# Performance work log

Hardware: AMD Instinct MI355X
Metric: run time of the kernel (lower is better)

## Reference

```python
import jax, jax.numpy as jnp
import numpy as np

N_NODES = 100000

def graph_conv(x, edge_index, w_root, w_rel, b):
    # PyG GraphConv (aggr='add'): out = aggr(x_j) @ W_rel + b + x @ W_root
    src, dst = edge_index[0], edge_index[1]
    msgs = x[src]                                   # [E, F_in] gather
    agg = jax.ops.segment_sum(msgs, dst, num_segments=N_NODES)  # [N, F_in] scatter-add
    return agg @ w_rel + b + x @ w_root             # [N, F_out]


def setup_inputs() -> dict:
    key = jax.random.key(0)
    ks = jax.random.split(key, 12)
    E = 1600000
    return {
        "x": jax.random.normal(ks[0], (N_NODES, 16), dtype=jnp.float32),
        "edge_index": jax.random.randint(ks[1], (2, E), 0, N_NODES, dtype=jnp.int64),
        "w_root1": jax.random.normal(ks[2], (16, 32), dtype=jnp.float32) * 0.1,
        "w_rel1": jax.random.normal(ks[3], (16, 32), dtype=jnp.float32) * 0.1,
        "b1": jax.random.normal(ks[4], (32,), dtype=jnp.float32) * 0.1,
        "w_root2": jax.random.normal(ks[5], (32, 64), dtype=jnp.float32) * 0.1,
        "w_rel2": jax.random.normal(ks[6], (32, 64), dtype=jnp.float32) * 0.1,
        "b2": jax.random.normal(ks[7], (64,), dtype=jnp.float32) * 0.1,
        "fc1_w": jax.random.normal(ks[8], (64, 32), dtype=jnp.float32) * 0.1,
        "fc1_b": jax.random.normal(ks[9], (32,), dtype=jnp.float32) * 0.1,
        "fc2_w": jax.random.normal(ks[10], (32, 16), dtype=jnp.float32) * 0.1,
        "fc2_b": jax.random.normal(ks[11], (16,), dtype=jnp.float32) * 0.1,
    }


def reference(x, edge_index, w_root1, w_rel1, b1, w_root2, w_rel2, b2,
              fc1_w, fc1_b, fc2_w, fc2_b):
    h = jax.nn.relu(graph_conv(x, edge_index, w_root1, w_rel1, b1))   # [N, 32]
    h = jax.nn.relu(graph_conv(h, edge_index, w_root2, w_rel2, b2))   # [N, 64]
    h = jax.nn.relu(h @ fc1_w + fc1_b)                                 # [N, 32]
    return h @ fc2_w + fc2_b                                           # [N, 16]
```

## Files before the change

### kernel.cpp

```cpp
#include <hip/hip_runtime.h>

#define F4E(v,i) ((i)==0?(v).x:((i)==1?(v).y:((i)==2?(v).z:(v).w)))

#define CHUNK 4096
#define ITERS 8

__device__ inline float4 shfl4b(float4 v, int src) {
    float4 r;
    r.x = __shfl(v.x, src, 4); r.y = __shfl(v.y, src, 4);
    r.z = __shfl(v.z, src, 4); r.w = __shfl(v.w, src, 4);
    return r;
}
__device__ inline float4 shfl8b(float4 v, int src) {
    float4 r;
    r.x = __shfl(v.x, src, 8); r.y = __shfl(v.y, src, 8);
    r.z = __shfl(v.z, src, 8); r.w = __shfl(v.w, src, 8);
    return r;
}

__global__ __launch_bounds__(512) void k_bhist(
    const int* __restrict__ ei, int* __restrict__ bhist, int E, int NB)
{
    __shared__ int cnt[512];
    int t = threadIdx.x;
    cnt[t] = 0;
    __syncthreads();
    int base = blockIdx.x * CHUNK;
#pragma unroll
    for (int i = 0; i < ITERS; ++i) {
        int e = base + i * 512 + t;
        if (e < E) {
            int dst = ei[E + e];
            atomicAdd(&cnt[dst >> 8], 1);
        }
    }
    __syncthreads();
    if (t < NB && cnt[t]) atomicAdd(&bhist[t], cnt[t]);
}

__global__ __launch_bounds__(512) void k_bscan(
    const int* __restrict__ bhist, int* __restrict__ bstart,
    int* __restrict__ gcursor, int NB, int E)
{
    __shared__ int s[512];
    int t = threadIdx.x;
    int v0 = (t < NB) ? bhist[t] : 0;
    s[t] = v0;
    __syncthreads();
    for (int off = 1; off < 512; off <<= 1) {
        int v = (t >= off) ? s[t - off] : 0;
        __syncthreads();
        s[t] += v;
        __syncthreads();
    }
    if (t < NB) { int ex = s[t] - v0; bstart[t] = ex; gcursor[t] = ex; }
    if (t == 0) bstart[NB] = E;
}

__global__ __launch_bounds__(512) void k_partition(
    const int* __restrict__ ei, int* __restrict__ gcursor,
    int* __restrict__ epack, int E)
{
    __shared__ int cnt[512], sc[512], lbase[512], gbase[512], lcnt[512];
    __shared__ int stage[CHUNK];
    __shared__ unsigned short stageb[CHUNK];
    int t = threadIdx.x;
    cnt[t] = 0; lcnt[t] = 0;
    __syncthreads();

    int base = blockIdx.x * CHUNK;
    int pk[ITERS], bb[ITERS];
#pragma unroll
    for (int i = 0; i < ITERS; ++i) {
        int e = base + i * 512 + t;
        if (e < E) {
            int src = ei[e], dst = ei[E + e];
            pk[i] = (src << 8) | (dst & 255);
            bb[i] = dst >> 8;
            atomicAdd(&cnt[bb[i]], 1);
        } else bb[i] = -1;
    }
    __syncthreads();

    int v0 = cnt[t];
    sc[t] = v0;
    __syncthreads();
    for (int off = 1; off < 512; off <<= 1) {
        int v = (t >= off) ? sc[t - off] : 0;
        __syncthreads();
        sc[t] += v;
        __syncthreads();
    }
    lbase[t] = sc[t] - v0;
    if (v0 > 0) gbase[t] = atomicAdd(&gcursor[t], v0);
    __syncthreads();

#pragma unroll
    for (int i = 0; i < ITERS; ++i) {
        if (bb[i] >= 0) {
            int loc = atomicAdd(&lcnt[bb[i]], 1);
            int slot = lbase[bb[i]] + loc;
            stage[slot] = pk[i];
            stageb[slot] = (unsigned short)bb[i];
        }
    }
    __syncthreads();

    int m = min(CHUNK, E - base);
#pragma unroll
    for (int i = 0; i < ITERS; ++i) {
        int slot = i * 512 + t;
        if (slot < m) {
            int b = stageb[slot];
            epack[gbase[b] + (slot - lbase[b])] = stage[slot];
        }
    }
}

__global__ __launch_bounds__(256) void k_sort(
    const int* __restrict__ bstart, const int* __restrict__ epack,
    int* __restrict__ rs, int* __restrict__ esorted, int N, int E)
{
    __shared__ int hist[256], cur[256], sc[256];
    int t = threadIdx.x;
    int b = blockIdx.x;
    int s0 = bstart[b], s1 = bstart[b + 1];
    hist[t] = 0;
    __syncthreads();
    for (int e = s0 + t; e < s1; e += 256)
        atomicAdd(&hist[epack[e] & 255], 1);
    __syncthreads();

    int v0 = hist[t];
    sc[t] = v0;
    __syncthreads();
    for (int off = 1; off < 256; off <<= 1) {
        int v = (t >= off) ? sc[t - off] : 0;
        __syncthreads();
        sc[t] += v;
        __syncthreads();
    }
    int excl = sc[t] - v0;
    cur[t] = excl;
    int node = (b << 8) + t;
    if (node < N) rs[node] = s0 + excl;
    if (b == 0 && t == 0) rs[N] = E;
    __syncthreads();

    for (int e = s0 + t; e < s1; e += 256) {
        int pk = epack[e];
        int dlo = pk & 255;
        int pos = s0 + atomicAdd(&cur[dlo], 1);
        esorted[pos] = ((unsigned)pk) >> 8;
    }
}

__global__ __launch_bounds__(256) void k_g1f(
    const float* __restrict__ x, const int* __restrict__ rs,
    const int* __restrict__ esrc,
    const float* __restrict__ wroot, const float* __restrict__ wrel,
    const float* __restrict__ bias, float* __restrict__ h1, int N)
{
    __shared__ float4 s_wr[128], s_wl[128], s_b[8];
    int t = threadIdx.x;
    if (t < 128) {
        s_wr[t] = reinterpret_cast<const float4*>(wroot)[t];
        s_wl[t] = reinterpret_cast<const float4*>(wrel)[t];
    }
    if (t < 8) s_b[t] = reinterpret_cast<const float4*>(bias)[t];
    __syncthreads();

    int tid = blockIdx.x * 256 + t;
    int n = tid >> 2, p = tid & 3;
    if (n >= N) return;
    int s0 = rs[n], s1 = rs[n + 1];
    float4 g = make_float4(0.f, 0.f, 0.f, 0.f);
    int e = s0;
    for (; e + 1 < s1; e += 2) {
        int src0 = esrc[e], src1 = esrc[e + 1];
        float4 v0 = *reinterpret_cast<const float4*>(x + (size_t)src0 * 16 + p * 4);
        float4 v1 = *reinterpret_cast<const float4*>(x + (size_t)src1 * 16 + p * 4);
        g.x += v0.x + v1.x; g.y += v0.y + v1.y;
        g.z += v0.z + v1.z; g.w += v0.w + v1.w;
    }
    if (e < s1) {
        int src0 = esrc[e];
        float4 v0 = *reinterpret_cast<const float4*>(x + (size_t)src0 * 16 + p * 4);
        g.x += v0.x; g.y += v0.y; g.z += v0.z; g.w += v0.w;
    }
    float4 a = *reinterpret_cast<const float4*>(x + (size_t)n * 16 + p * 4);

    int jb = p * 2;
    float4 acc0 = s_b[jb], acc1 = s_b[jb + 1];
#pragma unroll
    for (int kc = 0; kc < 4; ++kc) {
        float4 a4 = shfl4b(a, kc);
        float4 g4 = shfl4b(g, kc);
#pragma unroll
        for (int kk = 0; kk < 4; ++kk) {
            float av = F4E(a4, kk), gv = F4E(g4, kk);
            int k = kc * 4 + kk;
            float4 wr0 = s_wr[k * 8 + jb], wr1 = s_wr[k * 8 + jb + 1];
            float4 wl0 = s_wl[k * 8 + jb], wl1 = s_wl[k * 8 + jb + 1];
            acc0.x += av * wr0.x + gv * wl0.x;
            acc0.y += av * wr0.y + gv * wl0.y;
            acc0.z += av * wr0.z + gv * wl0.z;
            acc0.w += av * wr0.w + gv * wl0.w;
            acc1.x += av * wr1.x + gv * wl1.x;
            acc1.y += av * wr1.y + gv * wl1.y;
            acc1.z += av * wr1.z + gv * wl1.z;
            acc1.w += av * wr1.w + gv * wl1.w;
        }
    }
    acc0.x = fmaxf(acc0.x, 0.f); acc0.y = fmaxf(acc0.y, 0.f);
    acc0.z = fmaxf(acc0.z, 0.f); acc0.w = fmaxf(acc0.w, 0.f);
    acc1.x = fmaxf(acc1.x, 0.f); acc1.y = fmaxf(acc1.y, 0.f);
    acc1.z = fmaxf(acc1.z, 0.f); acc1.w = fmaxf(acc1.w, 0.f);
    float4* o = reinterpret_cast<float4*>(h1 + (size_t)n * 32 + p * 8);
    o[0] = acc0; o[1] = acc1;
}

__global__ __launch_bounds__(256) void k_g2f(
    const float* __restrict__ h1, const int* __restrict__ rs,
    const int* __restrict__ esrc,
    const float* __restrict__ wroot, const float* __restrict__ wrel,
    const float* __restrict__ bias,
    const float* __restrict__ f1w, const float* __restrict__ f1b,
    const float* __restrict__ f2w, const float* __restrict__ f2b,
    float* __restrict__ out, int N)
{
    __shared__ float4 s_wr[512], s_wl[512], s_b[16];
    __shared__ float4 s_f1[512];
    __shared__ float  s_f2[512];
    __shared__ float4 s_b1[8];
    __shared__ float  s_b2[16];
    int t = threadIdx.x;
    for (int i = t; i < 512; i += 256) {
        s_wr[i] = reinterpret_cast<const float4*>(wroot)[i];
        s_wl[i] = reinterpret_cast<const float4*>(wrel)[i];
        int k = i >> 3, jc = i & 7;
        s_f1[(i & ~7) | ((jc + (k >> 3)) & 7)] = reinterpret_cast<const float4*>(f1w)[i];
        s_f2[i] = f2w[i];
    }
    if (t < 16) s_b[t]  = reinterpret_cast<const float4*>(bias)[t];
    if (t < 8)  s_b1[t] = reinterpret_cast<const float4*>(f1b)[t];
    if (t < 16) s_b2[t] = f2b[t];
    __syncthreads();

    int tid = blockIdx.x * 256 + t;
    int n = tid >> 3, p = tid & 7;
    if (n >= N) return;

    int s0 = rs[n], s1 = rs[n + 1];
    float4 g = make_float4(0.f, 0.f, 0.f, 0.f);
    int e = s0;
    for (; e + 1 < s1; e += 2) {
        int src0 = esrc[e], src1 = esrc[e + 1];
        float4 v0 = *reinterpret_cast<const float4*>(h1 + (size_t)src0 * 32 + p * 4);
        float4 v1 = *reinterpret_cast<const float4*>(h1 + (size_t)src1 * 32 + p * 4);
        g.x += v0.x + v1.x; g.y += v0.y + v1.y;
        g.z += v0.z + v1.z; g.w += v0.w + v1.w;
    }
    if (e < s1) {
        int src0 = esrc[e];
        float4 v0 = *reinterpret_cast<const float4*>(h1 + (size_t)src0 * 32 + p * 4);
        g.x += v0.x; g.y += v0.y; g.z += v0.z; g.w += v0.w;
    }
    float4 a = *reinterpret_cast<const float4*>(h1 + (size_t)n * 32 + p * 4);

    int jb = p * 2;
    float4 acc0 = s_b[jb], acc1 = s_b[jb + 1];
#pragma unroll
    for (int kc = 0; kc < 8; ++kc) {
        float4 a4 = shfl8b(a, kc);
        float4 g4 = shfl8b(g, kc);
#pragma unroll
        for (int kk = 0; kk < 4; ++kk) {
            float av = F4E(a4, kk), gv = F4E(g4, kk);
            int k = kc * 4 + kk;
            float4 wr0 = s_wr[k * 16 + jb], wr1 = s_wr[k * 16 + jb + 1];
            float4 wl0 = s_wl[k * 16 + jb], wl1 = s_wl[k * 16 + jb + 1];
            acc0.x += av * wr0.x + gv * wl0.x;
            acc0.y += av * wr0.y + gv * wl0.y;
            acc0.z += av * wr0.z + gv * wl0.z;
            acc0.w += av * wr0.w + gv * wl0.w;
            acc1.x += av * wr1.x + gv * wl1.x;
            acc1.y += av * wr1.y + gv * wl1.y;
            acc1.z += av * wr1.z + gv * wl1.z;
            acc1.w += av * wr1.w + gv * wl1.w;
        }
    }
    acc0.x = fmaxf(acc0.x, 0.f); acc0.y = fmaxf(acc0.y, 0.f);
    acc0.z = fmaxf(acc0.z, 0.f); acc0.w = fmaxf(acc0.w, 0.f);
    acc1.x = fmaxf(acc1.x, 0.f); acc1.y = fmaxf(acc1.y, 0.f);
    acc1.z = fmaxf(acc1.z, 0.f); acc1.w = fmaxf(acc1.w, 0.f);

    float4 f[8];
    float4 z4 = make_float4(0.f, 0.f, 0.f, 0.f);
#pragma unroll
    for (int jc = 0; jc < 8; ++jc) f[jc] = p ? z4 : s_b1[jc];
#pragma unroll
    for (int kk = 0; kk < 8; ++kk) {
        float hv = (kk < 4) ? F4E(acc0, kk) : F4E(acc1, kk - 4);
        int k = p * 8 + kk;
        int row = k * 8;
#pragma unroll
        for (int jc = 0; jc < 8; ++jc) {
            float4 w = s_f1[row | ((jc + p) & 7)];
            f[jc].x += hv * w.x; f[jc].y += hv * w.y;
            f[jc].z += hv * w.z; f[jc].w += hv * w.w;
        }
    }
#pragma unroll
    for (int m = 1; m < 8; m <<= 1) {
#pragma unroll
        for (int jc = 0; jc < 8; ++jc) {
            f[jc].x += __shfl_xor(f[jc].x, m);
            f[jc].y += __shfl_xor(f[jc].y, m);
            f[jc].z += __shfl_xor(f[jc].z, m);
            f[jc].w += __shfl_xor(f[jc].w, m);
        }
    }
#pragma unroll
    for (int jc = 0; jc < 8; ++jc) {
        f[jc].x = fmaxf(f[jc].x, 0.f); f[jc].y = fmaxf(f[jc].y, 0.f);
        f[jc].z = fmaxf(f[jc].z, 0.f); f[jc].w = fmaxf(f[jc].w, 0.f);
    }

    float o0 = s_b2[p * 2], o1 = s_b2[p * 2 + 1];
#pragma unroll
    for (int k2 = 0; k2 < 32; ++k2) {
        float av = F4E(f[k2 >> 2], k2 & 3);
        o0 += av * s_f2[k2 * 16 + p * 2];
        o1 += av * s_f2[k2 * 16 + p * 2 + 1];
    }
    float2* o = reinterpret_cast<float2*>(out + (size_t)n * 16 + p * 2);
    *o = make_float2(o0, o1);
}

extern "C" void kernel_launch(void* const* d_in, const int* in_sizes, int n_in,
                              void* d_out, int out_size, void* d_ws, size_t ws_size,
                              hipStream_t stream)
{
    const float* x   = (const float*)d_in[0];
    const int*   ei  = (const int*)d_in[1];
    const float* wr1 = (const float*)d_in[2];
    const float* wl1 = (const float*)d_in[3];
    const float* b1  = (const float*)d_in[4];
    const float* wr2 = (const float*)d_in[5];
    const float* wl2 = (const float*)d_in[6];
    const float* b2  = (const float*)d_in[7];
    const float* f1w = (const float*)d_in[8];
    const float* f1b = (const float*)d_in[9];
    const float* f2w = (const float*)d_in[10];
    const float* f2b = (const float*)d_in[11];
    float* out = (float*)d_out;

    const int N  = in_sizes[0] / 16;
    const int E  = in_sizes[1] / 2;
    const int NB = (N + 255) >> 8;

    float* ws      = (float*)d_ws;
    float* h1      = ws;
    int*   esorted = (int*)(ws + (size_t)N * 32);
    int*   epack   = esorted + E;
    int*   rs      = epack + E;
    int*   bhist   = rs + N + 1;
    int*   bstart  = bhist + NB;
    int*   gcursor = bstart + NB + 1;

    hipMemsetAsync(bhist, 0, (size_t)NB * sizeof(int), stream);

    int nchunk = (E + CHUNK - 1) / CHUNK;
    int g_g1 = (N * 4 + 255) / 256;
    int g_g2 = (N * 8 + 255) / 256;

    k_bhist    <<<nchunk, 512, 0, stream>>>(ei, bhist, E, NB);
    k_bscan    <<<1,      512, 0, stream>>>(bhist, bstart, gcursor, NB, E);
    k_partition<<<nchunk, 512, 0, stream>>>(ei, gcursor, epack, E);
    k_sort     <<<NB,     256, 0, stream>>>(bstart, epack, rs, esorted, N, E);

    k_g1f      <<<g_g1, 256, 0, stream>>>(x, rs, esorted, wr1, wl1, b1, h1, N);
    k_g2f      <<<g_g2, 256, 0, stream>>>(h1, rs, esorted, wr2, wl2, b2,
                                          f1w, f1b, f2w, f2b, out, N);
}
```

Before: 229.5 us.

## Bin nodes by in-degree into a permutation to balance gather-loop work per wavefront

Counts node in-degrees into 64 bins during the per-bucket sort and adds a kernel that builds a degree-sorted node permutation. Both GraphConv kernels then walk nodes in that order, so lanes in a wavefront have similar loop trip counts and divergence drops. The gather loops are also unrolled from 2 to 4 edges to keep more loads in flight. In exchange it adds an extra kernel launch, global atomics on 64 counters, an indirection load per node, and scattered output writes and root-row reads because neighbouring threads no longer handle neighbouring nodes.

New measurement: 800.2 us. 3.49x slower.

```diff
diff --git a/kernel.cpp b/kernel.cpp
--- a/kernel.cpp
+++ b/kernel.cpp
@@ -119,7 +119,8 @@
 
 __global__ __launch_bounds__(256) void k_sort(
     const int* __restrict__ bstart, const int* __restrict__ epack,
-    int* __restrict__ rs, int* __restrict__ esorted, int N, int E)
+    int* __restrict__ rs, int* __restrict__ esorted,
+    int* __restrict__ dcnt, int N, int E)
 {
     __shared__ int hist[256], cur[256], sc[256];
     int t = threadIdx.x;
@@ -143,7 +144,10 @@
     int excl = sc[t] - v0;
     cur[t] = excl;
     int node = (b << 8) + t;
-    if (node < N) rs[node] = s0 + excl;
+    if (node < N) {
+        rs[node] = s0 + excl;
+        atomicAdd(&dcnt[min(v0, 63)], 1);
+    }
     if (b == 0 && t == 0) rs[N] = E;
     __syncthreads();
 
@@ -155,9 +159,34 @@
     }
 }
 
+__global__ __launch_bounds__(256) void k_perm(
+    const int* __restrict__ rs, const int* __restrict__ dcnt,
+    int* __restrict__ dcur, int* __restrict__ perm, int N)
+{
+    __shared__ int sstart[64];
+    int t = threadIdx.x;
+    if (t < 64) {
+        int v = dcnt[t];
+        int incl = v;
+#pragma unroll
+        for (int d = 1; d < 64; d <<= 1) {
+            int o = __shfl_up(incl, d, 64);
+            if (t >= d) incl += o;
+        }
+        sstart[t] = incl - v;
+    }
+    __syncthreads();
+    int node = blockIdx.x * 256 + t;
+    if (node >= N) return;
+    int deg = rs[node + 1] - rs[node];
+    int bin = min(deg, 63);
+    int pos = sstart[bin] + atomicAdd(&dcur[bin], 1);
+    perm[pos] = node;
+}
+
 __global__ __launch_bounds__(256) void k_g1f(
     const float* __restrict__ x, const int* __restrict__ rs,
-    const int* __restrict__ esrc,
+    const int* __restrict__ esrc, const int* __restrict__ perm,
     const float* __restrict__ wroot, const float* __restrict__ wrel,
     const float* __restrict__ bias, float* __restrict__ h1, int N)
 {
@@ -171,21 +200,26 @@
     __syncthreads();
 
     int tid = blockIdx.x * 256 + t;
-    int n = tid >> 2, p = tid & 3;
-    if (n >= N) return;
+    int q = tid >> 2, p = tid & 3;
+    if (q >= N) return;
+    int n = perm[q];
     int s0 = rs[n], s1 = rs[n + 1];
     float4 g = make_float4(0.f, 0.f, 0.f, 0.f);
     int e = s0;
-    for (; e + 1 < s1; e += 2) {
-        int src0 = esrc[e], src1 = esrc[e + 1];
-        float4 v0 = *reinterpret_cast<const float4*>(x + (size_t)src0 * 16 + p * 4);
-        float4 v1 = *reinterpret_cast<const float4*>(x + (size_t)src1 * 16 + p * 4);
-        g.x += v0.x + v1.x; g.y += v0.y + v1.y;
-        g.z += v0.z + v1.z; g.w += v0.w + v1.w;
-    }
-    if (e < s1) {
-        int src0 = esrc[e];
-        float4 v0 = *reinterpret_cast<const float4*>(x + (size_t)src0 * 16 + p * 4);
+    for (; e + 3 < s1; e += 4) {
+        int sa = esrc[e], sb = esrc[e + 1], sc = esrc[e + 2], sd = esrc[e + 3];
+        float4 v0 = *reinterpret_cast<const float4*>(x + (size_t)sa * 16 + p * 4);
+        float4 v1 = *reinterpret_cast<const float4*>(x + (size_t)sb * 16 + p * 4);
+        float4 v2 = *reinterpret_cast<const float4*>(x + (size_t)sc * 16 + p * 4);
+        float4 v3 = *reinterpret_cast<const float4*>(x + (size_t)sd * 16 + p * 4);
+        g.x += (v0.x + v1.x) + (v2.x + v3.x);
+        g.y += (v0.y + v1.y) + (v2.y + v3.y);
+        g.z += (v0.z + v1.z) + (v2.z + v3.z);
+        g.w += (v0.w + v1.w) + (v2.w + v3.w);
+    }
+    for (; e < s1; ++e) {
+        int sa = esrc[e];
+        float4 v0 = *reinterpret_cast<const float4*>(x + (size_t)sa * 16 + p * 4);
         g.x += v0.x; g.y += v0.y; g.z += v0.z; g.w += v0.w;
     }
     float4 a = *reinterpret_cast<const float4*>(x + (size_t)n * 16 + p * 4);
@@ -222,7 +256,7 @@
 
 __global__ __launch_bounds__(256) void k_g2f(
     const float* __restrict__ h1, const int* __restrict__ rs,
-    const int* __restrict__ esrc,
+    const int* __restrict__ esrc, const int* __restrict__ perm,
     const float* __restrict__ wroot, const float* __restrict__ wrel,
     const float* __restrict__ bias,
     const float* __restrict__ f1w, const float* __restrict__ f1b,
@@ -248,22 +282,27 @@
     __syncthreads();
 
     int tid = blockIdx.x * 256 + t;
-    int n = tid >> 3, p = tid & 7;
-    if (n >= N) return;
+    int q = tid >> 3, p = tid & 7;
+    if (q >= N) return;
+    int n = perm[q];
 
     int s0 = rs[n], s1 = rs[n + 1];
     float4 g = make_float4(0.f, 0.f, 0.f, 0.f);
     int e = s0;
-    for (; e + 1 < s1; e += 2) {
-        int src0 = esrc[e], src1 = esrc[e + 1];
-        float4 v0 = *reinterpret_cast<const float4*>(h1 + (size_t)src0 * 32 + p * 4);
-        float4 v1 = *reinterpret_cast<const float4*>(h1 + (size_t)src1 * 32 + p * 4);
-        g.x += v0.x + v1.x; g.y += v0.y + v1.y;
-        g.z += v0.z + v1.z; g.w += v0.w + v1.w;
-    }
-    if (e < s1) {
-        int src0 = esrc[e];
-        float4 v0 = *reinterpret_cast<const float4*>(h1 + (size_t)src0 * 32 + p * 4);
+    for (; e + 3 < s1; e += 4) {
+        int sa = esrc[e], sb = esrc[e + 1], sc = esrc[e + 2], sd = esrc[e + 3];
+        float4 v0 = *reinterpret_cast<const float4*>(h1 + (size_t)sa * 32 + p * 4);
+        float4 v1 = *reinterpret_cast<const float4*>(h1 + (size_t)sb * 32 + p * 4);
+        float4 v2 = *reinterpret_cast<const float4*>(h1 + (size_t)sc * 32 + p * 4);
+        float4 v3 = *reinterpret_cast<const float4*>(h1 + (size_t)sd * 32 + p * 4);
+        g.x += (v0.x + v1.x) + (v2.x + v3.x);
+        g.y += (v0.y + v1.y) + (v2.y + v3.y);
+        g.z += (v0.z + v1.z) + (v2.z + v3.z);
+        g.w += (v0.w + v1.w) + (v2.w + v3.w);
+    }
+    for (; e < s1; ++e) {
+        int sa = esrc[e];
+        float4 v0 = *reinterpret_cast<const float4*>(h1 + (size_t)sa * 32 + p * 4);
         g.x += v0.x; g.y += v0.y; g.z += v0.z; g.w += v0.w;
     }
     float4 a = *reinterpret_cast<const float4*>(h1 + (size_t)n * 32 + p * 4);
@@ -366,21 +405,28 @@
     int*   epack   = esorted + E;
     int*   rs      = epack + E;
     int*   bhist   = rs + N + 1;
-    int*   bstart  = bhist + NB;
+    int*   dcnt    = bhist + NB;
+    int*   dcur    = dcnt + 64;
+    int*   bstart  = dcur + 64;
     int*   gcursor = bstart + NB + 1;
-
-    hipMemsetAsync(bhist, 0, (size_t)NB * sizeof(int), stream);
+    int*   perm    = gcursor + NB;
+
+    hipMemsetAsync(bhist, 0, (size_t)(NB + 128) * sizeof(int), stream);
 
     int nchunk = (E + CHUNK - 1) / CHUNK;
+    int g_n  = (N + 255) / 256;
     int g_g1 = (N * 4 + 255) / 256;
     int g_g2 = (N * 8 + 255) / 256;
 
     k_bhist    <<<nchunk, 512, 0, stream>>>(ei, bhist, E, NB);
     k_bscan    <<<1,      512, 0, stream>>>(bhist, bstart, gcursor, NB, E);
     k_partition<<<nchunk, 512, 0, stream>>>(ei, gcursor, epack, E);
-    k_sort     <<<NB,     256, 0, stream>>>(bstart, epack, rs, esorted, N, E);
-
-    k_g1f      <<<g_g1, 256, 0, stream>>>(x, rs, esorted, wr1, wl1, b1, h1, N);
-    k_g2f      <<<g_g2, 256, 0, stream>>>(h1, rs, esorted, wr2, wl2, b2,
+    k_sort     <<<NB,     256, 0, stream>>>(bstart, epack, rs, esorted, dcnt, N, E);
+    k_perm     <<<g_n,    256, 0, stream>>>(rs, dcnt, dcur, perm, N);
+
+    k_g1f      <<<g_g1, 256, 0, stream>>>(x, rs, esorted, perm,
+                                          wr1, wl1, b1, h1, N);
+    k_g2f      <<<g_g2, 256, 0, stream>>>(h1, rs, esorted, perm,
+                                          wr2, wl2, b2,
                                           f1w, f1b, f2w, f2b, out, N);
 }
```

## Store intermediate h1 as bf16 and unroll gather loops by eight

Applied to the files above, without the earlier changes.

The layer-1 output h1 is now written as packed bf16 with round-to-nearest-even, which halves the bytes the layer-2 gather reads per edge. Both gather loops are unrolled to issue eight independent loads before accumulating, to raise memory-level parallelism. The cost is lost precision in h1 and more registers per thread, which could reduce occupancy.

Result: faster. 220.6 us (-3.9%).

```diff
diff --git a/kernel.cpp b/kernel.cpp
--- a/kernel.cpp
+++ b/kernel.cpp
@@ -17,6 +17,15 @@
     r.z = __shfl(v.z, src, 8); r.w = __shfl(v.w, src, 8);
     return r;
 }
+
+__device__ inline unsigned packbf2(float a, float b) {
+    unsigned ua = __float_as_uint(a), ub = __float_as_uint(b);
+    ua = (ua + 0x7fffu + ((ua >> 16) & 1u)) >> 16;
+    ub = (ub + 0x7fffu + ((ub >> 16) & 1u)) >> 16;
+    return ua | (ub << 16);
+}
+__device__ inline float bflo(unsigned w) { return __uint_as_float(w << 16); }
+__device__ inline float bfhi(unsigned w) { return __uint_as_float(w & 0xffff0000u); }
 
 __global__ __launch_bounds__(512) void k_bhist(
     const int* __restrict__ ei, int* __restrict__ bhist, int E, int NB)
@@ -159,7 +168,7 @@
     const float* __restrict__ x, const int* __restrict__ rs,
     const int* __restrict__ esrc,
     const float* __restrict__ wroot, const float* __restrict__ wrel,
-    const float* __restrict__ bias, float* __restrict__ h1, int N)
+    const float* __restrict__ bias, unsigned short* __restrict__ h1, int N)
 {
     __shared__ float4 s_wr[128], s_wl[128], s_b[8];
     int t = threadIdx.x;
@@ -176,16 +185,21 @@
     int s0 = rs[n], s1 = rs[n + 1];
     float4 g = make_float4(0.f, 0.f, 0.f, 0.f);
     int e = s0;
-    for (; e + 1 < s1; e += 2) {
-        int src0 = esrc[e], src1 = esrc[e + 1];
-        float4 v0 = *reinterpret_cast<const float4*>(x + (size_t)src0 * 16 + p * 4);
-        float4 v1 = *reinterpret_cast<const float4*>(x + (size_t)src1 * 16 + p * 4);
-        g.x += v0.x + v1.x; g.y += v0.y + v1.y;
-        g.z += v0.z + v1.z; g.w += v0.w + v1.w;
-    }
-    if (e < s1) {
-        int src0 = esrc[e];
-        float4 v0 = *reinterpret_cast<const float4*>(x + (size_t)src0 * 16 + p * 4);
+    for (; e + 7 < s1; e += 8) {
+        float4 v[8];
+#pragma unroll
+        for (int u = 0; u < 8; ++u) {
+            int src = esrc[e + u];
+            v[u] = *reinterpret_cast<const float4*>(x + (size_t)src * 16 + p * 4);
+        }
+#pragma unroll
+        for (int u = 0; u < 8; ++u) {
+            g.x += v[u].x; g.y += v[u].y; g.z += v[u].z; g.w += v[u].w;
+        }
+    }
+    for (; e < s1; ++e) {
+        int src = esrc[e];
+        float4 v0 = *reinterpret_cast<const float4*>(x + (size_t)src * 16 + p * 4);
         g.x += v0.x; g.y += v0.y; g.z += v0.z; g.w += v0.w;
     }
     float4 a = *reinterpret_cast<const float4*>(x + (size_t)n * 16 + p * 4);
@@ -216,12 +230,17 @@
     acc0.z = fmaxf(acc0.z, 0.f); acc0.w = fmaxf(acc0.w, 0.f);
     acc1.x = fmaxf(acc1.x, 0.f); acc1.y = fmaxf(acc1.y, 0.f);
     acc1.z = fmaxf(acc1.z, 0.f); acc1.w = fmaxf(acc1.w, 0.f);
-    float4* o = reinterpret_cast<float4*>(h1 + (size_t)n * 32 + p * 8);
-    o[0] = acc0; o[1] = acc1;
+
+    uint4 w;
+    w.x = packbf2(acc0.x, acc0.y);
+    w.y = packbf2(acc0.z, acc0.w);
+    w.z = packbf2(acc1.x, acc1.y);
+    w.w = packbf2(acc1.z, acc1.w);
+    reinterpret_cast<uint4*>(h1 + (size_t)n * 32)[p] = w;
 }
 
 __global__ __launch_bounds__(256) void k_g2f(
-    const float* __restrict__ h1, const int* __restrict__ rs,
+    const unsigned short* __restrict__ h1, const int* __restrict__ rs,
     const int* __restrict__ esrc,
     const float* __restrict__ wroot, const float* __restrict__ wrel,
     const float* __restrict__ bias,
@@ -254,19 +273,27 @@
     int s0 = rs[n], s1 = rs[n + 1];
     float4 g = make_float4(0.f, 0.f, 0.f, 0.f);
     int e = s0;
-    for (; e + 1 < s1; e += 2) {
-        int src0 = esrc[e], src1 = esrc[e + 1];
-        float4 v0 = *reinterpret_cast<const float4*>(h1 + (size_t)src0 * 32 + p * 4);
-        float4 v1 = *reinterpret_cast<const float4*>(h1 + (size_t)src1 * 32 + p * 4);
-        g.x += v0.x + v1.x; g.y += v0.y + v1.y;
-        g.z += v0.z + v1.z; g.w += v0.w + v1.w;
-    }
-    if (e < s1) {
-        int src0 = esrc[e];
-        float4 v0 = *reinterpret_cast<const float4*>(h1 + (size_t)src0 * 32 + p * 4);
-        g.x += v0.x; g.y += v0.y; g.z += v0.z; g.w += v0.w;
-    }
-    float4 a = *reinterpret_cast<const float4*>(h1 + (size_t)n * 32 + p * 4);
+    for (; e + 7 < s1; e += 8) {
+        uint2 w[8];
+#pragma unroll
+        for (int u = 0; u < 8; ++u) {
+            int src = esrc[e + u];
+            w[u] = reinterpret_cast<const uint2*>(h1 + (size_t)src * 32)[p];
+        }
+#pragma unroll
+        for (int u = 0; u < 8; ++u) {
+            g.x += bflo(w[u].x); g.y += bfhi(w[u].x);
+            g.z += bflo(w[u].y); g.w += bfhi(w[u].y);
+        }
+    }
+    for (; e < s1; ++e) {
+        int src = esrc[e];
+        uint2 w0 = reinterpret_cast<const uint2*>(h1 + (size_t)src * 32)[p];
+        g.x += bflo(w0.x); g.y += bfhi(w0.x);
+        g.z += bflo(w0.y); g.w += bfhi(w0.y);
+    }
+    uint2 aw = reinterpret_cast<const uint2*>(h1 + (size_t)n * 32)[p];
+    float4 a = make_float4(bflo(aw.x), bfhi(aw.x), bflo(aw.y), bfhi(aw.y));
 
     int jb = p * 2;
     float4 acc0 = s_b[jb], acc1 = s_b[jb + 1];
@@ -360,14 +387,14 @@
     const int E  = in_sizes[1] / 2;
     const int NB = (N + 255) >> 8;
 
-    float* ws      = (float*)d_ws;
-    float* h1      = ws;
-    int*   esorted = (int*)(ws + (size_t)N * 32);
-    int*   epack   = esorted + E;
-    int*   rs      = epack + E;
-    int*   bhist   = rs + N + 1;
-    int*   bstart  = bhist + NB;
-    int*   gcursor = bstart + NB + 1;
+    float*          ws      = (float*)d_ws;
+    unsigned short* h1      = (unsigned short*)ws;
+    int*            esorted = (int*)(ws + (size_t)N * 16);
+    int*            epack   = esorted + E;
+    int*            rs      = epack + E;
+    int*            bhist   = rs + N + 1;
+    int*            bstart  = bhist + NB;
+    int*            gcursor = bstart + NB + 1;
 
     hipMemsetAsync(bhist, 0, (size_t)NB * sizeof(int), stream);
 
```
